# Optimization experiments

Measured on AMD Instinct MI355X. Metric: run time of the kernel, lower is better.

The kernel has to match this reference:

```python
import jax, jax.numpy as jnp
import numpy as np

B, S, LD, Hh, Ww = 64, 32, 16, 32, 18
D, NH, HD, FF, L = 512, 8, 64, 2048, 6
IN = LD * Hh * Ww  # 9216
EPS = 1e-5


def setup_inputs() -> dict:
    key = jax.random.key(0)
    ks = jax.random.split(key, 8)
    p = lambda k, s: jax.random.normal(k, s, jnp.float32) * 0.02
    return {
        "x": jax.random.normal(ks[0], (B, S, LD, Hh, Ww), jnp.float32),
        "inp_w": p(ks[1], (D, IN)), "inp_b": jnp.zeros((D,), jnp.float32),
        "in_proj_w": p(ks[2], (L, 3 * D, D)), "in_proj_b": jnp.zeros((L, 3 * D), jnp.float32),
        "out_w": p(ks[3], (L, D, D)), "out_b": jnp.zeros((L, D), jnp.float32),
        "ln1_w": jnp.ones((L, D), jnp.float32), "ln1_b": jnp.zeros((L, D), jnp.float32),
        "ln2_w": jnp.ones((L, D), jnp.float32), "ln2_b": jnp.zeros((L, D), jnp.float32),
        "ff1_w": p(ks[4], (L, FF, D)), "ff1_b": jnp.zeros((L, FF), jnp.float32),
        "ff2_w": p(ks[5], (L, D, FF)), "ff2_b": jnp.zeros((L, D), jnp.float32),
        "outp_w": p(ks[6], (IN, D)), "outp_b": jnp.zeros((IN,), jnp.float32),
    }


def _layernorm(x, w, b):
    mu = jnp.mean(x, -1, keepdims=True)
    var = jnp.mean(jnp.square(x - mu), -1, keepdims=True)
    return (x - mu) * jax.lax.rsqrt(var + EPS) * w + b


def _rope(x, cos, sin):
    # x: [B,S,NH,HD]; torchtune interleaved-pair rotation, rope applied BEFORE qk projection
    x2 = x.reshape(*x.shape[:-1], HD // 2, 2)
    x0, x1 = x2[..., 0], x2[..., 1]
    c = cos[None, :, None, :]
    s = sin[None, :, None, :]
    out = jnp.stack([x0 * c - x1 * s, x1 * c + x0 * s], axis=-1)
    return out.reshape(x.shape)


def reference(x, inp_w, inp_b, in_proj_w, in_proj_b, out_w, out_b,
              ln1_w, ln1_b, ln2_w, ln2_b, ff1_w, ff1_b, ff2_w, ff2_b,
              outp_w, outp_b):
    b, s = x.shape[0], x.shape[1]
    h = x.reshape(b, s, IN) @ inp_w.T + inp_b  # [B,S,D]

    theta = 1.0 / (10000.0 ** (jnp.arange(0, HD, 2, dtype=jnp.float32) / HD))
    ang = jnp.arange(s, dtype=jnp.float32)[:, None] * theta  # [S, HD/2]
    cos, sin = jnp.cos(ang), jnp.sin(ang)
    mask = jnp.triu(jnp.full((s, s), -jnp.inf, jnp.float32), k=1)  # causal additive mask
    scale = 1.0 / np.sqrt(HD)

    for i in range(L):
        # RoPE on full hidden state (pre-projection), used for q and k; v uses unrotated h
        hr = _rope(h.reshape(b, s, NH, HD), cos, sin).reshape(b, s, D)
        wq, wk, wv = in_proj_w[i, :D], in_proj_w[i, D:2 * D], in_proj_w[i, 2 * D:]
        bq, bk, bv = in_proj_b[i, :D], in_proj_b[i, D:2 * D], in_proj_b[i, 2 * D:]
        q = (hr @ wq.T + bq).reshape(b, s, NH, HD)
        k = (hr @ wk.T + bk).reshape(b, s, NH, HD)
        v = (h @ wv.T + bv).reshape(b, s, NH, HD)
        scores = jnp.einsum('bqhd,bkhd->bhqk', q, k) * scale + mask
        attn = jax.nn.softmax(scores, axis=-1)
        ctx = jnp.einsum('bhqk,bkhd->bqhd', attn, v).reshape(b, s, D)
        sa = ctx @ out_w[i].T + out_b[i]
        h = _layernorm(h + sa, ln1_w[i], ln1_b[i])  # post-norm (norm_first=False)
        ff = jax.nn.gelu(h @ ff1_w[i].T + ff1_b[i], approximate=False) @ ff2_w[i].T + ff2_b[i]
        h = _layernorm(h + ff, ln2_w[i], ln2_b[i])

    out = h @ outp_w.T + outp_b
    return out.reshape(b, s, LD, Hh, Ww)
```

## Files before the change

kernel.cpp:

```cpp
#include <hip/hip_runtime.h>
#include <hip/hip_bf16.h>
#include <math.h>


typedef __attribute__((ext_vector_type(8))) short bf16x8;
typedef __attribute__((ext_vector_type(4))) short bf16x4;
typedef __attribute__((ext_vector_type(8))) float f32x8;
typedef __attribute__((ext_vector_type(4))) float f32x4;

#define LN_EPS 1e-5f

__device__ inline float bf2f(__hip_bfloat16 v) { return __bfloat162float(v); }
__device__ inline __hip_bfloat16 f2bf(float f) { return __float2bfloat16(f); }

__device__ __forceinline__ void gload_lds16(const __hip_bfloat16* g, __hip_bfloat16* l) {
    __builtin_amdgcn_global_load_lds(
        (const __attribute__((address_space(1))) unsigned*)g,
        (__attribute__((address_space(3))) unsigned*)l, 16, 0, 0);
}

__device__ __forceinline__ void sync_tile() {
    asm volatile("s_waitcnt vmcnt(0) lgkmcnt(0)" ::: "memory");
    __builtin_amdgcn_s_barrier();
    asm volatile("" ::: "memory");
}

__global__ __launch_bounds__(1024) void rope_prep(float* __restrict__ tab) {
    const int t = threadIdx.x;
    const int s = t >> 5, p = t & 31;
    const float theta = powf(10000.f, -(float)p / 32.f);
    float sn, cs;
    sincosf((float)s * theta, &sn, &cs);
    tab[t * 2] = cs;
    tab[t * 2 + 1] = sn;
}

struct CvtSeg { const float* src; __hip_bfloat16* dst; };
struct CvtArgs { CvtSeg seg[16]; long cum[17]; };

__global__ __launch_bounds__(256) void convert_all(CvtArgs a, long total8) {
    for (long i = (long)blockIdx.x * 256 + threadIdx.x; i < total8;
         i += (long)gridDim.x * 256) {
        int s = 0;
        while (i >= a.cum[s + 1]) ++s;
        const long off = i - a.cum[s];
        const f32x8 x = *((const f32x8*)a.seg[s].src + off);
        union { bf16x8 v; __hip_bfloat16 b[8]; } o;
#pragma unroll
        for (int t = 0; t < 8; ++t) o.b[t] = f2bf(x[t]);
        *((bf16x8*)a.seg[s].dst + off) = o.v;
    }
}

template<int BM, int BN, int EPI, int OUT, int AMODE, int SWZ>
__global__ __launch_bounds__(256) void gemm_bt(
    const void* __restrict__ Araw, int bn_split,
    const float* __restrict__ rtab,
    const __hip_bfloat16* __restrict__ W,
    const __hip_bfloat16* __restrict__ bias,
    void* __restrict__ Cv,
    int M, int N, int Ktot, int KC)
{
    constexpr int FM = BM / 32, FN = BN / 32;
    constexpr int CPT_A = BM / 32, CPT_B = BN / 32;
    __shared__ __align__(16) __hip_bfloat16 sA[BM * 64];
    __shared__ __align__(16) __hip_bfloat16 sB[BN * 64];

    const int tid = threadIdx.x, lane = tid & 63, wave = tid >> 6;
    const int wr = wave >> 1, wc = wave & 1;
    const int lr = lane & 15, lk = lane >> 4;

    int bm, bn, zz;
    if (SWZ == 0) {
        const int nbm = gridDim.x, nbn = gridDim.y;
        const int nwg = nbm * nbn;
        const int orig = blockIdx.y * nbm + blockIdx.x;
        const int q8 = nwg >> 3, r8 = nwg & 7;
        const int xcd = orig & 7, loc = orig >> 3;
        const int f = (xcd < r8 ? xcd * (q8 + 1) : r8 * (q8 + 1) + (xcd - r8) * q8) + loc;
        bm = f % nbm; bn = f / nbm; zz = blockIdx.z;
    } else {
        const int bid = blockIdx.x;
        const int xcd = bid & 7, loc = bid >> 3;
        const int nbn = N / BN;
        const int per = (gridDim.x >> 3) / nbn;
        bn = loc % nbn;
        const int gid = xcd * per + loc / nbn;
        bm = gid % (M / BM); zz = gid / (M / BM);
    }
    const int kbeg = zz * KC, kend = kbeg + KC;
    const bool dorot = (AMODE == 2) && (bn < bn_split);

    const __hip_bfloat16* Ab = (const __hip_bfloat16*)Araw + (long)bm * BM * Ktot;
    const float*          Af = (const float*)Araw + (long)bm * BM * Ktot;
    const __hip_bfloat16* Wb = W + (long)bn * BN * Ktot;

    f32x4 acc[FM][FN];
#pragma unroll
    for (int i = 0; i < FM; ++i)
#pragma unroll
        for (int j = 0; j < FN; ++j) acc[i][j] = (f32x4){0.f, 0.f, 0.f, 0.f};

    f32x8  aregf[CPT_A];
    bf16x8 aregb[CPT_A];
    f32x8  csreg[CPT_A];

    auto stageA_g = [&](int k0) {
#pragma unroll
        for (int c = 0; c < CPT_A; ++c) {
            const int ch = tid + c * 256, row = ch >> 3, co = ch & 7;
            gload_lds16(&Ab[(long)row * Ktot + k0 + ((co ^ (row & 7)) * 8)],
                        (__hip_bfloat16*)((char*)sA + ch * 16));
        }
    };
    auto stageB_g = [&](int k0) {
#pragma unroll
        for (int c = 0; c < CPT_B; ++c) {
            const int ch = tid + c * 256, row = ch >> 3, co = ch & 7;
            gload_lds16(&Wb[(long)row * Ktot + k0 + ((co ^ (row & 7)) * 8)],
                        (__hip_bfloat16*)((char*)sB + ch * 16));
        }
    };
    auto issueA = [&](int k0) {
#pragma unroll
        for (int c = 0; c < CPT_A; ++c) {
            const int ch = tid + c * 256, row = ch >> 3, co = ch & 7;
            if (AMODE == 1) aregf[c] = *(const f32x8*)&Af[(long)row * Ktot + k0 + co * 8];
            if (AMODE == 2) {
                aregb[c] = *(const bf16x8*)&Ab[(long)row * Ktot + k0 + co * 8];
                if (dorot)
                    csreg[c] = *(const f32x8*)&rtab[((bm * BM + row) & 31) * 64 + co * 8];
            }
        }
    };
    auto writeA = [&]() {
#pragma unroll
        for (int c = 0; c < CPT_A; ++c) {
            const int ch = tid + c * 256, row = ch >> 3, co = ch & 7;
            union { bf16x8 v; __hip_bfloat16 b[8]; } t;
            if (AMODE == 1) {
#pragma unroll
                for (int j = 0; j < 8; ++j) t.b[j] = f2bf(aregf[c][j]);
            } else {
                t.v = aregb[c];
                if (dorot) {
#pragma unroll
                    for (int qd = 0; qd < 4; ++qd) {
                        const float c_ = csreg[c][qd * 2], sn = csreg[c][qd * 2 + 1];
                        const float x0 = bf2f(t.b[2 * qd]);
                        const float x1 = bf2f(t.b[2 * qd + 1]);
                        t.b[2 * qd]     = f2bf(x0 * c_ - x1 * sn);
                        t.b[2 * qd + 1] = f2bf(x1 * c_ + x0 * sn);
                    }
                }
            }
            *(bf16x8*)((char*)sA + row * 128 + ((co ^ (row & 7)) << 4)) = t.v;
        }
    };
    auto compute = [&]() {
        bf16x8 af[2][FM], bfr[2][FN];
#pragma unroll
        for (int ks = 0; ks < 2; ++ks) {
#pragma unroll
            for (int i = 0; i < FM; ++i) {
                const int row = wr * (BM / 2) + i * 16 + lr;
                const int co = ks * 4 + lk;
                af[ks][i] = *(const bf16x8*)((const char*)sA + row * 128 +
                                             ((co ^ (row & 7)) << 4));
            }
#pragma unroll
            for (int j = 0; j < FN; ++j) {
                const int row = wc * (BN / 2) + j * 16 + lr;
                const int co = ks * 4 + lk;
                bfr[ks][j] = *(const bf16x8*)((const char*)sB + row * 128 +
                                              ((co ^ (row & 7)) << 4));
            }
        }
#pragma unroll
        for (int ks = 0; ks < 2; ++ks)
#pragma unroll
            for (int i = 0; i < FM; ++i)
#pragma unroll
                for (int j = 0; j < FN; ++j)
                    acc[i][j] = __builtin_amdgcn_mfma_f32_16x16x32_bf16(
                        af[ks][i], bfr[ks][j], acc[i][j], 0, 0, 0);
    };

    if (AMODE != 0) issueA(kbeg);
    for (int k0 = kbeg; k0 < kend; k0 += 64) {
        if (k0 > kbeg) __builtin_amdgcn_s_barrier();
        if (AMODE == 0) stageA_g(k0);
        stageB_g(k0);
        if (AMODE != 0) writeA();
        sync_tile();
        if (AMODE != 0 && k0 + 64 < kend) issueA(k0 + 64);
        compute();
    }

    const int row0 = bm * BM + wr * (BM / 2);
    const int col0 = bn * BN + wc * (BN / 2);
    if (OUT == 1) {
        float* Cp = (float*)Cv + (long)zz * M * N;
#pragma unroll
        for (int i = 0; i < FM; ++i)
#pragma unroll
            for (int j = 0; j < FN; ++j) {
                const int col = col0 + j * 16 + lr;
#pragma unroll
                for (int r = 0; r < 4; ++r)
                    Cp[(long)(row0 + i * 16 + lk * 4 + r) * N + col] = acc[i][j][r];
            }
    } else {
#pragma unroll
        for (int i = 0; i < FM; ++i)
#pragma unroll
            for (int j = 0; j < FN; ++j) {
                const int col = col0 + j * 16 + lr;
                const float bv = bf2f(bias[col]);
#pragma unroll
                for (int r = 0; r < 4; ++r) {
                    const int row = row0 + i * 16 + lk * 4 + r;
                    float v = acc[i][j][r] + bv;
                    if (EPI == 1) v = 0.5f * v * (1.0f + erff(v * 0.70710678118654752f));
                    const long idx = (long)row * N + col;
                    if (OUT == 2) ((float*)Cv)[idx] = v;
                    else          ((__hip_bfloat16*)Cv)[idx] = f2bf(v);
                }
            }
    }
}

__global__ __launch_bounds__(256) void sk_reduce_rt(
    const float* __restrict__ part, const __hip_bfloat16* __restrict__ bias,
    __hip_bfloat16* __restrict__ out, int SK)
{
    const long MN = 2048L * 512;
    const long i4 = ((long)blockIdx.x * 256 + threadIdx.x) * 4;
    f32x4 s = (f32x4){0.f, 0.f, 0.f, 0.f};
    for (int z = 0; z < SK; ++z) s += *(const f32x4*)&part[z * MN + i4];
    const int col = (int)(i4 & 511);
    union { bf16x4 v; __hip_bfloat16 b[4]; } o;
#pragma unroll
    for (int j = 0; j < 4; ++j) o.b[j] = f2bf(s[j] + bf2f(bias[col + j]));
    *(bf16x4*)&out[i4] = o.v;
}

template<int SK>
__global__ __launch_bounds__(256) void skred_add_ln(
    const float* __restrict__ part, const __hip_bfloat16* __restrict__ bias,
    const __hip_bfloat16* __restrict__ resid,
    const __hip_bfloat16* __restrict__ w, const __hip_bfloat16* __restrict__ b,
    __hip_bfloat16* __restrict__ out)
{
    const long MN = 2048L * 512;
    const int wave = threadIdx.x >> 6, lane = threadIdx.x & 63;
    const long row = (long)blockIdx.x * 4 + wave;
    const long base = row * 512 + lane * 8;

    f32x8 acc = *(const f32x8*)&part[base];
#pragma unroll
    for (int z = 1; z < SK; ++z) acc += *(const f32x8*)&part[z * MN + base];

    union { bf16x8 v; __hip_bfloat16 b[8]; } ur, uo;
    ur.v = *(const bf16x8*)&resid[base];

    float x[8];
    float s = 0.f, s2 = 0.f;
#pragma unroll
    for (int j = 0; j < 8; ++j) {
        const int col = lane * 8 + j;
        x[j] = acc[j] + bf2f(bias[col]) + bf2f(ur.b[j]);
        s += x[j];
        s2 += x[j] * x[j];
    }
#pragma unroll
    for (int off = 32; off; off >>= 1) {
        s  += __shfl_xor(s, off);
        s2 += __shfl_xor(s2, off);
    }
    const float mu = s * (1.f / 512.f);
    const float var = s2 * (1.f / 512.f) - mu * mu;
    const float rs = rsqrtf(var + LN_EPS);
#pragma unroll
    for (int j = 0; j < 8; ++j) {
        const int col = lane * 8 + j;
        uo.b[j] = f2bf((x[j] - mu) * rs * bf2f(w[col]) + bf2f(b[col]));
    }
    *(bf16x8*)&out[base] = uo.v;
}

__global__ __launch_bounds__(256) void attn_mfma(
    const __hip_bfloat16* __restrict__ qkv, __hip_bfloat16* __restrict__ ctx)
{
    __shared__ __align__(16) __hip_bfloat16 sP[4][32 * 32];
    __shared__ __align__(16) __hip_bfloat16 sVT[4][64 * 32];

    const int wave = threadIdx.x >> 6, lane = threadIdx.x & 63;
    const int bh = blockIdx.x * 4 + wave;
    const int b = bh >> 3, head = bh & 7;
    const long tok0 = (long)b * 32;
    const int lr = lane & 15, lk = lane >> 4;

    const __hip_bfloat16* Qb = qkv + tok0 * 1536 + head * 64;
    const __hip_bfloat16* Kb = Qb + 512;
    const __hip_bfloat16* Vb = Qb + 1024;

#pragma unroll
    for (int t = 0; t < 4; ++t) {
        const int c = lane + t * 64, row = c >> 3, d0 = (c & 7) * 8;
        union { bf16x8 v; __hip_bfloat16 e[8]; } u;
        u.v = *(const bf16x8*)&Vb[(long)row * 1536 + d0];
#pragma unroll
        for (int e = 0; e < 8; ++e) sVT[wave][(d0 + e) * 32 + row] = u.e[e];
    }

    f32x4 sc[2][2];
#pragma unroll
    for (int i = 0; i < 2; ++i)
#pragma unroll
        for (int j = 0; j < 2; ++j) sc[i][j] = (f32x4){0.f, 0.f, 0.f, 0.f};
#pragma unroll
    for (int ks = 0; ks < 2; ++ks) {
        bf16x8 aq[2], bk[2];
#pragma unroll
        for (int i = 0; i < 2; ++i)
            aq[i] = *(const bf16x8*)&Qb[(long)(i * 16 + lr) * 1536 + ks * 32 + lk * 8];
#pragma unroll
        for (int j = 0; j < 2; ++j)
            bk[j] = *(const bf16x8*)&Kb[(long)(j * 16 + lr) * 1536 + ks * 32 + lk * 8];
#pragma unroll
        for (int i = 0; i < 2; ++i)
#pragma unroll
            for (int j = 0; j < 2; ++j)
                sc[i][j] = __builtin_amdgcn_mfma_f32_16x16x32_bf16(aq[i], bk[j], sc[i][j], 0, 0, 0);
    }

    float p[2][2][4], inv[2][4];
#pragma unroll
    for (int i = 0; i < 2; ++i) {
#pragma unroll
        for (int r = 0; r < 4; ++r) {
            const int row = i * 16 + lk * 4 + r;
            float m = -3.0e38f;
#pragma unroll
            for (int j = 0; j < 2; ++j) {
                const int col = j * 16 + lr;
                const float v = (col <= row) ? sc[i][j][r] * 0.125f : -3.0e38f;
                p[i][j][r] = v;
                m = fmaxf(m, v);
            }
#pragma unroll
            for (int off = 1; off < 16; off <<= 1)
                m = fmaxf(m, __shfl_xor(m, off));
            float l = 0.f;
#pragma unroll
            for (int j = 0; j < 2; ++j) {
                p[i][j][r] = expf(p[i][j][r] - m);
                l += p[i][j][r];
            }
#pragma unroll
            for (int off = 1; off < 16; off <<= 1)
                l += __shfl_xor(l, off);
            inv[i][r] = 1.f / l;
        }
    }

#pragma unroll
    for (int i = 0; i < 2; ++i)
#pragma unroll
        for (int j = 0; j < 2; ++j)
#pragma unroll
            for (int r = 0; r < 4; ++r)
                sP[wave][(i * 16 + lk * 4 + r) * 32 + j * 16 + lr] = f2bf(p[i][j][r]);

    bf16x8 pa[2], vb[4];
#pragma unroll
    for (int i = 0; i < 2; ++i)
        pa[i] = *(const bf16x8*)&sP[wave][(i * 16 + lr) * 32 + lk * 8];
#pragma unroll
    for (int j = 0; j < 4; ++j)
        vb[j] = *(const bf16x8*)&sVT[wave][(j * 16 + lr) * 32 + lk * 8];

    f32x4 o[2][4];
#pragma unroll
    for (int i = 0; i < 2; ++i)
#pragma unroll
        for (int j = 0; j < 4; ++j) {
            o[i][j] = (f32x4){0.f, 0.f, 0.f, 0.f};
            o[i][j] = __builtin_amdgcn_mfma_f32_16x16x32_bf16(pa[i], vb[j], o[i][j], 0, 0, 0);
        }

#pragma unroll
    for (int i = 0; i < 2; ++i)
#pragma unroll
        for (int j = 0; j < 4; ++j) {
            const int col = j * 16 + lr;
#pragma unroll
            for (int r = 0; r < 4; ++r) {
                const int row = i * 16 + lk * 4 + r;
                ctx[(tok0 + row) * 512 + head * 64 + col] = f2bf(o[i][j][r] * inv[i][r]);
            }
        }
}

extern "C" void kernel_launch(void* const* d_in, const int* in_sizes, int n_in,
                              void* d_out, int out_size, void* d_ws, size_t ws_size,
                              hipStream_t stream)
{
    const int M = 2048;
    __hip_bfloat16* wts = (__hip_bfloat16*)d_ws;

    const long O_INPW   = 0;
    const long O_INPROJ = 4718592;
    const long O_OUTW   = 9437184;
    const long O_FF1    = 11010048;
    const long O_FF2    = 17301504;
    const long O_OUTPW  = 23592960;
    const long O_INPB   = 28311552;
    const long O_INPROJB= 28312064;
    const long O_OUTB   = 28321280;
    const long O_LN1W   = 28324352;
    const long O_LN1B   = 28327424;
    const long O_LN2W   = 28330496;
    const long O_LN2B   = 28333568;
    const long O_FF1B   = 28336640;
    const long O_FF2B   = 28348928;
    const long O_OUTPB  = 28352000;
    const long O_ACT    = 28361216;

    __hip_bfloat16* h   = wts + O_ACT;
    __hip_bfloat16* ht  = h   + (long)M * 512;
    __hip_bfloat16* qkv = ht  + (long)M * 512;
    __hip_bfloat16* ctx = qkv + (long)M * 1536;
    __hip_bfloat16* ffh = ctx + (long)M * 512;
    float* rtab = (float*)(ffh + (long)M * 2048);
    float* skpart = (float*)((__hip_bfloat16*)rtab + 4096);

    const long skpart_byte_off = (char*)skpart - (char*)d_ws;
    const int zin = (ws_size >= (size_t)skpart_byte_off + 16L * M * 512 * 4) ? 16 : 8;

    rope_prep<<<1, 1024, 0, stream>>>(rtab);

    const int  cidx[16] = {1, 3, 5, 11, 13, 15, 2, 4, 6, 7, 8, 9, 10, 12, 14, 16};
    const long coff[16] = {O_INPW, O_INPROJ, O_OUTW, O_FF1, O_FF2, O_OUTPW,
                           O_INPB, O_INPROJB, O_OUTB, O_LN1W, O_LN1B, O_LN2W,
                           O_LN2B, O_FF1B, O_FF2B, O_OUTPB};
    const long csz[16]  = {4718592, 4718592, 1572864, 6291456, 6291456, 4718592,
                           512, 9216, 3072, 3072, 3072, 3072, 3072, 12288, 3072, 9216};
    CvtArgs ca;
    long cum = 0;
    for (int s = 0; s < 16; ++s) {
        ca.seg[s].src = (const float*)d_in[cidx[s]];
        ca.seg[s].dst = wts + coff[s];
        ca.cum[s] = cum;
        cum += csz[s] / 8;
    }
    ca.cum[16] = cum;
    convert_all<<<2048, 256, 0, stream>>>(ca, cum);

    gemm_bt<128, 128, 0, 1, 1, 1><<<64 * zin, 256, 0, stream>>>(
        d_in[0], 0, rtab, wts + O_INPW, wts + O_INPB, skpart, M, 512, 9216, 9216 / zin);
    sk_reduce_rt<<<1024, 256, 0, stream>>>(skpart, wts + O_INPB, h, zin);

    for (int i = 0; i < 6; ++i) {
        const __hip_bfloat16* wqkv = wts + O_INPROJ + (long)i * 1536 * 512;
        const __hip_bfloat16* bqkv = wts + O_INPROJB + i * 1536;

        gemm_bt<64, 64, 0, 0, 2, 0><<<dim3(32, 24), 256, 0, stream>>>(
            h, 16, rtab, wqkv, bqkv, qkv, M, 1536, 512, 512);
        attn_mfma<<<128, 256, 0, stream>>>(qkv, ctx);
        gemm_bt<64, 64, 0, 1, 0, 0><<<dim3(32, 8, 2), 256, 0, stream>>>(
            ctx, 0, rtab, wts + O_OUTW + (long)i * 512 * 512, wts + O_OUTB + i * 512,
            skpart, M, 512, 512, 256);
        skred_add_ln<2><<<512, 256, 0, stream>>>(
            skpart, wts + O_OUTB + i * 512, h,
            wts + O_LN1W + i * 512, wts + O_LN1B + i * 512, ht);
        gemm_bt<64, 64, 1, 0, 0, 0><<<dim3(32, 32), 256, 0, stream>>>(
            ht, 0, rtab, wts + O_FF1 + (long)i * 2048 * 512, wts + O_FF1B + i * 2048,
            ffh, M, 2048, 512, 512);
        gemm_bt<64, 64, 0, 1, 0, 0><<<dim3(32, 8, 4), 256, 0, stream>>>(
            ffh, 0, rtab, wts + O_FF2 + (long)i * 512 * 2048, wts + O_FF2B + i * 512,
            skpart, M, 512, 2048, 512);
        skred_add_ln<4><<<512, 256, 0, stream>>>(
            skpart, wts + O_FF2B + i * 512, ht,
            wts + O_LN2W + i * 512, wts + O_LN2B + i * 512, h);
    }

    gemm_bt<128, 128, 0, 2, 0, 0><<<dim3(16, 72), 256, 0, stream>>>(
        h, 0, rtab, wts + O_OUTPW, wts + O_OUTPB, d_out, M, 9216, 512, 512);
}
```

Baseline: 524.9 us.

## Double-buffer GEMM LDS, fuse attention with out-projection, retune split-K and tiles

The GEMM main loop now uses double-buffered shared-memory tiles, so loads for the next K step overlap compute on the current one. Attention is fused with the output projection: each 64-thread block computes one (batch, head), multiplies its context by that head's slice of out_w, and writes per-head partials that skred_add_ln<8> then reduces. This removes the ctx buffer round-trip and one GEMM launch, at the cost of 8x partial-sum traffic. The input projection is fixed at split-K 8 with a templated reducer, and the final projection switches to 64x64 tiles.

Result: slower. 599.8 us (+14.3%).

```diff
diff --git a/kernel.cpp b/kernel.cpp
--- a/kernel.cpp
+++ b/kernel.cpp
@@ -63,8 +63,8 @@
 {
     constexpr int FM = BM / 32, FN = BN / 32;
     constexpr int CPT_A = BM / 32, CPT_B = BN / 32;
-    __shared__ __align__(16) __hip_bfloat16 sA[BM * 64];
-    __shared__ __align__(16) __hip_bfloat16 sB[BN * 64];
+    __shared__ __align__(16) __hip_bfloat16 sA[2][BM * 64];
+    __shared__ __align__(16) __hip_bfloat16 sB[2][BN * 64];
 
     const int tid = threadIdx.x, lane = tid & 63, wave = tid >> 6;
     const int wr = wave >> 1, wc = wave & 1;
@@ -105,20 +105,20 @@
     bf16x8 aregb[CPT_A];
     f32x8  csreg[CPT_A];
 
-    auto stageA_g = [&](int k0) {
+    auto stageA_g = [&](int buf, int k0) {
 #pragma unroll
         for (int c = 0; c < CPT_A; ++c) {
             const int ch = tid + c * 256, row = ch >> 3, co = ch & 7;
             gload_lds16(&Ab[(long)row * Ktot + k0 + ((co ^ (row & 7)) * 8)],
-                        (__hip_bfloat16*)((char*)sA + ch * 16));
+                        (__hip_bfloat16*)((char*)&sA[buf][0] + ch * 16));
         }
     };
-    auto stageB_g = [&](int k0) {
+    auto stageB_g = [&](int buf, int k0) {
 #pragma unroll
         for (int c = 0; c < CPT_B; ++c) {
             const int ch = tid + c * 256, row = ch >> 3, co = ch & 7;
             gload_lds16(&Wb[(long)row * Ktot + k0 + ((co ^ (row & 7)) * 8)],
-                        (__hip_bfloat16*)((char*)sB + ch * 16));
+                        (__hip_bfloat16*)((char*)&sB[buf][0] + ch * 16));
         }
     };
     auto issueA = [&](int k0) {
@@ -133,7 +133,7 @@
             }
         }
     };
-    auto writeA = [&]() {
+    auto writeA = [&](int buf) {
 #pragma unroll
         for (int c = 0; c < CPT_A; ++c) {
             const int ch = tid + c * 256, row = ch >> 3, co = ch & 7;
@@ -154,10 +154,10 @@
                     }
                 }
             }
-            *(bf16x8*)((char*)sA + row * 128 + ((co ^ (row & 7)) << 4)) = t.v;
+            *(bf16x8*)((char*)&sA[buf][0] + row * 128 + ((co ^ (row & 7)) << 4)) = t.v;
         }
     };
-    auto compute = [&]() {
+    auto compute = [&](int buf) {
         bf16x8 af[2][FM], bfr[2][FN];
 #pragma unroll
         for (int ks = 0; ks < 2; ++ks) {
@@ -165,14 +165,14 @@
             for (int i = 0; i < FM; ++i) {
                 const int row = wr * (BM / 2) + i * 16 + lr;
                 const int co = ks * 4 + lk;
-                af[ks][i] = *(const bf16x8*)((const char*)sA + row * 128 +
+                af[ks][i] = *(const bf16x8*)((const char*)&sA[buf][0] + row * 128 +
                                              ((co ^ (row & 7)) << 4));
             }
 #pragma unroll
             for (int j = 0; j < FN; ++j) {
                 const int row = wc * (BN / 2) + j * 16 + lr;
                 const int co = ks * 4 + lk;
-                bfr[ks][j] = *(const bf16x8*)((const char*)sB + row * 128 +
+                bfr[ks][j] = *(const bf16x8*)((const char*)&sB[buf][0] + row * 128 +
                                               ((co ^ (row & 7)) << 4));
             }
         }
@@ -186,15 +186,27 @@
                         af[ks][i], bfr[ks][j], acc[i][j], 0, 0, 0);
     };
 
-    if (AMODE != 0) issueA(kbeg);
+    if (AMODE == 0) stageA_g(0, kbeg); else issueA(kbeg);
+    stageB_g(0, kbeg);
+    if (AMODE != 0) {
+        asm volatile("s_waitcnt vmcnt(0)" ::: "memory");
+        writeA(0);
+    }
+    sync_tile();
+
+    int cur = 0;
     for (int k0 = kbeg; k0 < kend; k0 += 64) {
-        if (k0 > kbeg) __builtin_amdgcn_s_barrier();
-        if (AMODE == 0) stageA_g(k0);
-        stageB_g(k0);
-        if (AMODE != 0) writeA();
-        sync_tile();
-        if (AMODE != 0 && k0 + 64 < kend) issueA(k0 + 64);
-        compute();
+        const bool hn = (k0 + 64 < kend);
+        if (hn) {
+            if (AMODE == 0) stageA_g(cur ^ 1, k0 + 64); else issueA(k0 + 64);
+            stageB_g(cur ^ 1, k0 + 64);
+        }
+        compute(cur);
+        if (hn) {
+            if (AMODE != 0) writeA(cur ^ 1);
+            sync_tile();
+        }
+        cur ^= 1;
     }
 
     const int row0 = bm * BM + wr * (BM / 2);
@@ -230,13 +242,15 @@
     }
 }
 
-__global__ __launch_bounds__(256) void sk_reduce_rt(
+template<int SK>
+__global__ __launch_bounds__(256) void sk_reduce(
     const float* __restrict__ part, const __hip_bfloat16* __restrict__ bias,
-    __hip_bfloat16* __restrict__ out, int SK)
+    __hip_bfloat16* __restrict__ out)
 {
     const long MN = 2048L * 512;
     const long i4 = ((long)blockIdx.x * 256 + threadIdx.x) * 4;
     f32x4 s = (f32x4){0.f, 0.f, 0.f, 0.f};
+#pragma unroll
     for (int z = 0; z < SK; ++z) s += *(const f32x4*)&part[z * MN + i4];
     const int col = (int)(i4 & 511);
     union { bf16x4 v; __hip_bfloat16 b[4]; } o;
@@ -289,15 +303,18 @@
     *(bf16x8*)&out[base] = uo.v;
 }
 
-__global__ __launch_bounds__(256) void attn_mfma(
-    const __hip_bfloat16* __restrict__ qkv, __hip_bfloat16* __restrict__ ctx)
+__global__ __launch_bounds__(64) void attn_out(
+    const __hip_bfloat16* __restrict__ qkv,
+    const __hip_bfloat16* __restrict__ outw,
+    float* __restrict__ part)
 {
-    __shared__ __align__(16) __hip_bfloat16 sP[4][32 * 32];
-    __shared__ __align__(16) __hip_bfloat16 sVT[4][64 * 32];
-
-    const int wave = threadIdx.x >> 6, lane = threadIdx.x & 63;
-    const int bh = blockIdx.x * 4 + wave;
+    __shared__ __align__(16) __hip_bfloat16 sP[32 * 32];
+    __shared__ __align__(16) __hip_bfloat16 sVT[64 * 32];
+    __shared__ __align__(16) __hip_bfloat16 sCtx[32 * 64];
+
+    const int bh = blockIdx.x;
     const int b = bh >> 3, head = bh & 7;
+    const int lane = threadIdx.x;
     const long tok0 = (long)b * 32;
     const int lr = lane & 15, lk = lane >> 4;
 
@@ -311,7 +328,7 @@
         union { bf16x8 v; __hip_bfloat16 e[8]; } u;
         u.v = *(const bf16x8*)&Vb[(long)row * 1536 + d0];
 #pragma unroll
-        for (int e = 0; e < 8; ++e) sVT[wave][(d0 + e) * 32 + row] = u.e[e];
+        for (int e = 0; e < 8; ++e) sVT[(d0 + e) * 32 + row] = u.e[e];
     }
 
     f32x4 sc[2][2];
@@ -371,15 +388,15 @@
         for (int j = 0; j < 2; ++j)
 #pragma unroll
             for (int r = 0; r < 4; ++r)
-                sP[wave][(i * 16 + lk * 4 + r) * 32 + j * 16 + lr] = f2bf(p[i][j][r]);
+                sP[(i * 16 + lk * 4 + r) * 32 + j * 16 + lr] = f2bf(p[i][j][r]);
 
     bf16x8 pa[2], vb[4];
 #pragma unroll
     for (int i = 0; i < 2; ++i)
-        pa[i] = *(const bf16x8*)&sP[wave][(i * 16 + lr) * 32 + lk * 8];
+        pa[i] = *(const bf16x8*)&sP[(i * 16 + lr) * 32 + lk * 8];
 #pragma unroll
     for (int j = 0; j < 4; ++j)
-        vb[j] = *(const bf16x8*)&sVT[wave][(j * 16 + lr) * 32 + lk * 8];
+        vb[j] = *(const bf16x8*)&sVT[(j * 16 + lr) * 32 + lk * 8];
 
     f32x4 o[2][4];
 #pragma unroll
@@ -393,14 +410,49 @@
 #pragma unroll
     for (int i = 0; i < 2; ++i)
 #pragma unroll
-        for (int j = 0; j < 4; ++j) {
-            const int col = j * 16 + lr;
-#pragma unroll
-            for (int r = 0; r < 4; ++r) {
-                const int row = i * 16 + lk * 4 + r;
-                ctx[(tok0 + row) * 512 + head * 64 + col] = f2bf(o[i][j][r] * inv[i][r]);
-            }
-        }
+        for (int j = 0; j < 4; ++j)
+#pragma unroll
+            for (int r = 0; r < 4; ++r)
+                sCtx[(i * 16 + lk * 4 + r) * 64 + j * 16 + lr] = f2bf(o[i][j][r] * inv[i][r]);
+    asm volatile("s_waitcnt lgkmcnt(0)" ::: "memory");
+
+    bf16x8 pa2[2][2];
+#pragma unroll
+    for (int ks = 0; ks < 2; ++ks)
+#pragma unroll
+        for (int i = 0; i < 2; ++i)
+            pa2[ks][i] = *(const bf16x8*)&sCtx[(i * 16 + lr) * 64 + ks * 32 + lk * 8];
+
+    const __hip_bfloat16* Wh = outw + head * 64;
+    float* Ph = part + (long)head * 2048 * 512;
+#pragma unroll
+    for (int jc = 0; jc < 4; ++jc) {
+        f32x4 a2[2][8];
+#pragma unroll
+        for (int i = 0; i < 2; ++i)
+#pragma unroll
+            for (int jj = 0; jj < 8; ++jj) a2[i][jj] = (f32x4){0.f, 0.f, 0.f, 0.f};
+#pragma unroll
+        for (int jj = 0; jj < 8; ++jj) {
+            const int j = jc * 8 + jj;
+#pragma unroll
+            for (int ks = 0; ks < 2; ++ks) {
+                const bf16x8 wf = *(const bf16x8*)&Wh[(long)(j * 16 + lr) * 512 + ks * 32 + lk * 8];
+#pragma unroll
+                for (int i = 0; i < 2; ++i)
+                    a2[i][jj] = __builtin_amdgcn_mfma_f32_16x16x32_bf16(pa2[ks][i], wf, a2[i][jj], 0, 0, 0);
+            }
+        }
+#pragma unroll
+        for (int i = 0; i < 2; ++i)
+#pragma unroll
+            for (int jj = 0; jj < 8; ++jj) {
+                const int col = (jc * 8 + jj) * 16 + lr;
+#pragma unroll
+                for (int r = 0; r < 4; ++r)
+                    Ph[(tok0 + i * 16 + lk * 4 + r) * 512 + col] = a2[i][jj][r];
+            }
+    }
 }
 
 extern "C" void kernel_launch(void* const* d_in, const int* in_sizes, int n_in,
@@ -431,13 +483,9 @@
     __hip_bfloat16* h   = wts + O_ACT;
     __hip_bfloat16* ht  = h   + (long)M * 512;
     __hip_bfloat16* qkv = ht  + (long)M * 512;
-    __hip_bfloat16* ctx = qkv + (long)M * 1536;
-    __hip_bfloat16* ffh = ctx + (long)M * 512;
+    __hip_bfloat16* ffh = qkv + (long)M * 1536;
     float* rtab = (float*)(ffh + (long)M * 2048);
     float* skpart = (float*)((__hip_bfloat16*)rtab + 4096);
-
-    const long skpart_byte_off = (char*)skpart - (char*)d_ws;
-    const int zin = (ws_size >= (size_t)skpart_byte_off + 16L * M * 512 * 4) ? 16 : 8;
 
     rope_prep<<<1, 1024, 0, stream>>>(rtab);
 
@@ -458,9 +506,9 @@
     ca.cum[16] = cum;
     convert_all<<<2048, 256, 0, stream>>>(ca, cum);
 
-    gemm_bt<128, 128, 0, 1, 1, 1><<<64 * zin, 256, 0, stream>>>(
-        d_in[0], 0, rtab, wts + O_INPW, wts + O_INPB, skpart, M, 512, 9216, 9216 / zin);
-    sk_reduce_rt<<<1024, 256, 0, stream>>>(skpart, wts + O_INPB, h, zin);
+    gemm_bt<128, 128, 0, 1, 1, 1><<<512, 256, 0, stream>>>(
+        d_in[0], 0, rtab, wts + O_INPW, wts + O_INPB, skpart, M, 512, 9216, 1152);
+    sk_reduce<8><<<1024, 256, 0, stream>>>(skpart, wts + O_INPB, h);
 
     for (int i = 0; i < 6; ++i) {
         const __hip_bfloat16* wqkv = wts + O_INPROJ + (long)i * 1536 * 512;
@@ -468,11 +516,9 @@
 
         gemm_bt<64, 64, 0, 0, 2, 0><<<dim3(32, 24), 256, 0, stream>>>(
             h, 16, rtab, wqkv, bqkv, qkv, M, 1536, 512, 512);
-        attn_mfma<<<128, 256, 0, stream>>>(qkv, ctx);
-        gemm_bt<64, 64, 0, 1, 0, 0><<<dim3(32, 8, 2), 256, 0, stream>>>(
-            ctx, 0, rtab, wts + O_OUTW + (long)i * 512 * 512, wts + O_OUTB + i * 512,
-            skpart, M, 512, 512, 256);
-        skred_add_ln<2><<<512, 256, 0, stream>>>(
+        attn_out<<<512, 64, 0, stream>>>(
+            qkv, wts + O_OUTW + (long)i * 512 * 512, skpart);
+        skred_add_ln<8><<<512, 256, 0, stream>>>(
             skpart, wts + O_OUTB + i * 512, h,
             wts + O_LN1W + i * 512, wts + O_LN1B + i * 512, ht);
         gemm_bt<64, 64, 1, 0, 0, 0><<<dim3(32, 32), 256, 0, stream>>>(
@@ -486,6 +532,6 @@
             wts + O_LN2W + i * 512, wts + O_LN2B + i * 512, h);
     }
 
-    gemm_bt<128, 128, 0, 2, 0, 0><<<dim3(16, 72), 256, 0, stream>>>(
+    gemm_bt<64, 64, 0, 2, 0, 0><<<dim3(32, 144), 256, 0, stream>>>(
         h, 0, rtab, wts + O_OUTPW, wts + O_OUTPB, d_out, M, 9216, 512, 512);
 }
```
